# Kernel tuning notes

Hardware: AMD Instinct MI355X
Metric: run time of the kernel (lower is better)

Reference implementation:

```python
import jax, jax.numpy as jnp
import numpy as np

B, T, D_IN, P, Q, D_OUT = 128, 1024, 64, 128, 2, 64


def _lstm_layer(x, w_ih, w_hh, b):
    """One LSTM layer, batch_first. x: [B,T,Din], w_ih: [4P,Din], w_hh: [4P,P], b: [4P].
    PyTorch gate order: i, f, g, o."""
    # Precompute input contribution for all timesteps (the big, parallel GEMM).
    gx = jnp.einsum('btd,gd->btg', x, w_ih) + b          # [B,T,4P]
    gx_t = jnp.swapaxes(gx, 0, 1)                        # [T,B,4P] for scan
    p = w_hh.shape[1]
    h0 = jnp.zeros((x.shape[0], p), dtype=x.dtype)
    c0 = jnp.zeros((x.shape[0], p), dtype=x.dtype)

    def step(carry, g_in):
        h, c = carry
        g = g_in + h @ w_hh.T                            # [B,4P]
        i, f, gg, o = jnp.split(g, 4, axis=-1)
        i = jax.nn.sigmoid(i)
        f = jax.nn.sigmoid(f)
        gg = jnp.tanh(gg)
        o = jax.nn.sigmoid(o)
        c = f * c + i * gg
        h = o * jnp.tanh(c)
        return (h, c), h

    _, hs = jax.lax.scan(step, (h0, c0), gx_t)           # hs: [T,B,P]
    return jnp.swapaxes(hs, 0, 1)                        # [B,T,P]


def setup_inputs() -> dict:
    key = jax.random.key(0)
    ks = jax.random.split(key, 8)
    x = jax.random.normal(ks[0], (B, T, D_IN), dtype=jnp.float32)
    # weight_ih: kaiming-normal-ish; weight_hh: orthogonal-ish (random normal is a fine stand-in
    # numerically; init distribution doesn't change the math being tested).
    w_ih0 = jax.random.normal(ks[1], (4 * P, D_IN), dtype=jnp.float32) * (1.0 / np.sqrt(D_IN))
    w_hh0 = jax.random.normal(ks[2], (4 * P, P), dtype=jnp.float32) * (1.0 / np.sqrt(P))
    w_ih1 = jax.random.normal(ks[3], (4 * P, P), dtype=jnp.float32) * (1.0 / np.sqrt(P))
    w_hh1 = jax.random.normal(ks[4], (4 * P, P), dtype=jnp.float32) * (1.0 / np.sqrt(P))
    # biases initialized to zero in the original (bias_ih + bias_hh folded into one per layer
    # would be equivalent math; keep both for faithfulness)
    b_ih = jnp.zeros((Q, 4 * P), dtype=jnp.float32)
    b_hh = jnp.zeros((Q, 4 * P), dtype=jnp.float32)
    fc_w = jax.random.normal(ks[5], (D_OUT, P), dtype=jnp.float32) * np.sqrt(2.0 / P)
    fc_b = jnp.zeros((D_OUT,), dtype=jnp.float32)
    return {"x": x, "w_ih0": w_ih0, "w_hh0": w_hh0, "w_ih1": w_ih1, "w_hh1": w_hh1,
            "b_ih": b_ih, "b_hh": b_hh, "fc_w": fc_w, "fc_b": fc_b}


def reference(x, w_ih0, w_hh0, w_ih1, w_hh1, b_ih, b_hh, fc_w, fc_b):
    h = _lstm_layer(x, w_ih0, w_hh0, b_ih[0] + b_hh[0])   # layer 0: [B,T,P]
    h = _lstm_layer(h, w_ih1, w_hh1, b_ih[1] + b_hh[1])   # layer 1: [B,T,P]
    return jnp.einsum('btp,op->bto', h, fc_w) + fc_b      # [B,T,D_OUT]
```

## Files before the change

kernel.cpp:

```cpp
#include <hip/hip_runtime.h>

#define NT 1024
#define RINGS 256

typedef _Float16 half8 __attribute__((ext_vector_type(8)));
typedef _Float16 half4 __attribute__((ext_vector_type(4)));
typedef float f32x4 __attribute__((ext_vector_type(4)));
typedef unsigned long long u64;
struct U2 { u64 a, b; };

#ifndef __has_builtin
#define __has_builtin(x) 0
#endif

__device__ __forceinline__ f32x4 MFMA(half8 a, half8 b, f32x4 c) {
  return __builtin_amdgcn_mfma_f32_16x16x32_f16(a, b, c, 0, 0, 0);
}
__device__ __forceinline__ float exp2h(float x) {
#if __has_builtin(__builtin_amdgcn_exp2f)
  return __builtin_amdgcn_exp2f(x);
#else
  return exp2f(x);
#endif
}
__device__ __forceinline__ float sigf(float x) {
  return __builtin_amdgcn_rcpf(1.0f + exp2h(x * -1.44269504f));
}
__device__ __forceinline__ float tanhf2(float x) {
  float t = __builtin_amdgcn_rcpf(1.0f + exp2h(x * 2.88539008f));
  return fmaf(-2.0f, t, 1.0f);
}
__device__ __forceinline__ half8 cvt8(float4 c0, float4 c1) {
  half8 hv;
  hv[0] = (_Float16)c0.x; hv[1] = (_Float16)c0.y;
  hv[2] = (_Float16)c0.z; hv[3] = (_Float16)c0.w;
  hv[4] = (_Float16)c1.x; hv[5] = (_Float16)c1.y;
  hv[6] = (_Float16)c1.z; hv[7] = (_Float16)c1.w;
  return hv;
}
__device__ __forceinline__ half8 ldring(const _Float16* p) {
  const u64* q = (const u64*)p;
  U2 uu;
  uu.a = __hip_atomic_load(q, __ATOMIC_RELAXED, __HIP_MEMORY_SCOPE_AGENT);
  uu.b = __hip_atomic_load(q + 1, __ATOMIC_RELAXED, __HIP_MEMORY_SCOPE_AGENT);
  return __builtin_bit_cast(half8, uu);
}
__device__ __forceinline__ unsigned wpoll(unsigned* p, unsigned tgt,
                                          unsigned cached, int l) {
  unsigned c = cached;
  while (c < tgt) {
    unsigned pv = 0;
    if (l == 0)
      pv = __hip_atomic_load(p, __ATOMIC_ACQUIRE, __HIP_MEMORY_SCOPE_AGENT);
    c = (unsigned)__builtin_amdgcn_readfirstlane((int)pv);
    if (c < tgt) __builtin_amdgcn_s_sleep(2);
  }
  return c;
}

__global__ __launch_bounds__(256) void prep_x(const float* __restrict__ x,
                                              _Float16* __restrict__ Xf) {
  int t0 = blockIdx.x * 256 + threadIdx.x;
  int l = t0 & 63;
  int fid = t0 >> 6;
  int kt = fid & 1;
  int t = (fid >> 1) & (NT - 1);
  int g = fid >> 11;
  int bt = g * 16 + (l & 15);
  int kb = kt * 32 + (l >> 4) * 4;
  const float* src = x + ((size_t)bt * NT + (size_t)t) * 64 + kb;
  float4 v0 = *(const float4*)src;
  float4 v1 = *(const float4*)(src + 16);
  *(half8*)(Xf + (size_t)fid * 512 + l * 8) = cvt8(v0, v1);
}

__global__ __launch_bounds__(512, 1) void lstm_main(
    const float* __restrict__ wih0, const float* __restrict__ whh0,
    const float* __restrict__ wih1, const float* __restrict__ whh1,
    const float* __restrict__ bih, const float* __restrict__ bhh,
    const float* __restrict__ fcw, const float* __restrict__ fcb,
    const _Float16* __restrict__ Xf, _Float16* __restrict__ ringH0,
    unsigned* __restrict__ flags, float* __restrict__ out) {
  const int tid = threadIdx.x;
  const int w = tid >> 6, l = tid & 63;
  const int n = l & 15, lg = l >> 4;
  const bool producer = blockIdx.x < 8;
  const int g = blockIdx.x & 7;

  __shared__ _Float16 hfr[2][4][64][8];
  __shared__ _Float16 fcl[4][4][64][8];

  _Float16* ringG = ringH0 + (size_t)g * RINGS * 2048;
  unsigned* prog = flags + g * 16;
  unsigned* cons = flags + (8 + g) * 16;
  const half8 hz = {0, 0, 0, 0, 0, 0, 0, 0};

  if (producer) {
    half8 A[4][6];
    f32x4 bias[4];
#pragma unroll
    for (int q = 0; q < 4; ++q) {
      int row = (w + 8 * q) * 16 + n;
#pragma unroll
      for (int kt = 0; kt < 2; ++kt) {
        const float* wp = wih0 + (size_t)row * 64 + kt * 32 + lg * 4;
        A[q][kt] = cvt8(*(const float4*)wp, *(const float4*)(wp + 16));
      }
#pragma unroll
      for (int kt = 0; kt < 4; ++kt) {
        const float* wp = whh0 + (size_t)row * 128 + kt * 32 + lg * 4;
        A[q][2 + kt] = cvt8(*(const float4*)wp, *(const float4*)(wp + 16));
      }
      int rb = (w + 8 * q) * 16 + lg * 4;
      f32x4 bv;
#pragma unroll
      for (int r = 0; r < 4; ++r) bv[r] = bih[rb + r] + bhh[rb + r];
      bias[q] = bv;
    }
    if (tid < 256) ((half8*)&hfr[1][0][0][0])[tid] = hz;
    const _Float16* XfG = Xf + (size_t)g * NT * 1024;
    half8 x0 = *(const half8*)(XfG + l * 8);
    half8 x1 = *(const half8*)(XfG + 512 + l * 8);
    f32x4 cst = {0.f, 0.f, 0.f, 0.f};
    unsigned Cc = 0;
    __syncthreads();
    for (int s = 0; s < NT; ++s) {
      half8 xn0, xn1;
      if (s + 1 < NT) {
        const _Float16* p = XfG + (size_t)(s + 1) * 1024 + l * 8;
        xn0 = *(const half8*)p;
        xn1 = *(const half8*)(p + 512);
      }
      if (s >= 224 && (s & 31) == 0)
        Cc = wpoll(cons, (unsigned)(s - 192), Cc, l);
      const int rdk = (s + 1) & 1;
      half8 b2 = *(const half8*)&hfr[rdk][0][l][0];
      half8 b3 = *(const half8*)&hfr[rdk][1][l][0];
      half8 b4 = *(const half8*)&hfr[rdk][2][l][0];
      half8 b5 = *(const half8*)&hfr[rdk][3][l][0];
      f32x4 xc0 = {0.f, 0.f, 0.f, 0.f}, xc1 = xc0, xc2 = xc0, xc3 = xc0;
      xc0 = MFMA(A[0][0], x0, xc0); xc1 = MFMA(A[1][0], x0, xc1);
      xc2 = MFMA(A[2][0], x0, xc2); xc3 = MFMA(A[3][0], x0, xc3);
      xc0 = MFMA(A[0][1], x1, xc0); xc1 = MFMA(A[1][1], x1, xc1);
      xc2 = MFMA(A[2][1], x1, xc2); xc3 = MFMA(A[3][1], x1, xc3);
      f32x4 hc0 = bias[0], hc1 = bias[1], hc2 = bias[2], hc3 = bias[3];
      hc0 = MFMA(A[0][2], b2, hc0); hc1 = MFMA(A[1][2], b2, hc1);
      hc2 = MFMA(A[2][2], b2, hc2); hc3 = MFMA(A[3][2], b2, hc3);
      hc0 = MFMA(A[0][3], b3, hc0); hc1 = MFMA(A[1][3], b3, hc1);
      hc2 = MFMA(A[2][3], b3, hc2); hc3 = MFMA(A[3][3], b3, hc3);
      hc0 = MFMA(A[0][4], b4, hc0); hc1 = MFMA(A[1][4], b4, hc1);
      hc2 = MFMA(A[2][4], b4, hc2); hc3 = MFMA(A[3][4], b4, hc3);
      hc0 = MFMA(A[0][5], b5, hc0); hc1 = MFMA(A[1][5], b5, hc1);
      hc2 = MFMA(A[2][5], b5, hc2); hc3 = MFMA(A[3][5], b5, hc3);
      f32x4 acc0 = hc0 + xc0, acc1 = hc1 + xc1;
      f32x4 acc2 = hc2 + xc2, acc3 = hc3 + xc3;
      half4 hh;
#pragma unroll
      for (int r = 0; r < 4; ++r) {
        float iv = sigf(acc0[r]), fv = sigf(acc1[r]);
        float gv = tanhf2(acc2[r]), ov = sigf(acc3[r]);
        cst[r] = fv * cst[r] + iv * gv;
        hh[r] = (_Float16)(ov * tanhf2(cst[r]));
      }
      *(half4*)&hfr[s & 1][w >> 1][l][(w & 1) << 2] = hh;
      {
        u64 uh = __builtin_bit_cast(u64, hh);
        __hip_atomic_store(
            (u64*)(ringG + (size_t)(s & (RINGS - 1)) * 2048 +
                   (w >> 1) * 512 + l * 8 + (w & 1) * 4),
            uh, __ATOMIC_RELAXED, __HIP_MEMORY_SCOPE_AGENT);
      }
      asm volatile("s_waitcnt lgkmcnt(0)" ::: "memory");
      __builtin_amdgcn_sched_barrier(0);
      __builtin_amdgcn_s_barrier();
      __builtin_amdgcn_sched_barrier(0);
      if ((s & 31) == 31) {
        asm volatile("s_waitcnt vmcnt(0)" ::: "memory");
        __builtin_amdgcn_sched_barrier(0);
        __builtin_amdgcn_s_barrier();
        __builtin_amdgcn_sched_barrier(0);
        if (tid == 0)
          __hip_atomic_store(prog, (unsigned)(s + 1), __ATOMIC_RELEASE,
                             __HIP_MEMORY_SCOPE_AGENT);
      }
      x0 = xn0;
      x1 = xn1;
    }
  } else {
    half8 A[4][8];
    f32x4 bias[4], fcbv = {0.f, 0.f, 0.f, 0.f};
#pragma unroll
    for (int q = 0; q < 4; ++q) {
      int row = (w + 8 * q) * 16 + n;
#pragma unroll
      for (int kt = 0; kt < 4; ++kt) {
        const float* wp = wih1 + (size_t)row * 128 + kt * 32 + lg * 4;
        A[q][kt] = cvt8(*(const float4*)wp, *(const float4*)(wp + 16));
      }
#pragma unroll
      for (int kt = 0; kt < 4; ++kt) {
        const float* wp = whh1 + (size_t)row * 128 + kt * 32 + lg * 4;
        A[q][4 + kt] = cvt8(*(const float4*)wp, *(const float4*)(wp + 16));
      }
      int rb = (w + 8 * q) * 16 + lg * 4;
      f32x4 bv;
#pragma unroll
      for (int r = 0; r < 4; ++r)
        bv[r] = bih[512 + rb + r] + bhh[512 + rb + r];
      bias[q] = bv;
    }
    if (w < 4) {
      int frow = (w << 4) + n;
#pragma unroll
      for (int kt = 0; kt < 4; ++kt) {
        const float* wp = fcw + (size_t)frow * 128 + kt * 32 + lg * 4;
        *(half8*)&fcl[w][kt][l][0] =
            cvt8(*(const float4*)wp, *(const float4*)(wp + 16));
      }
      fcbv = *(const f32x4*)(fcb + (w << 4) + lg * 4);
    }
    if (tid < 256) ((half8*)&hfr[1][0][0][0])[tid] = hz;
    float* outG = out + (size_t)((g << 4) + n) * NT * 64 + (w << 4) + lg * 4;
    f32x4 cst = {0.f, 0.f, 0.f, 0.f};
    __syncthreads();
    unsigned Pc = wpoll(prog, 2u, 0u, l);
    half8 hA0 = ldring(ringG + l * 8);
    half8 hA1 = ldring(ringG + 512 + l * 8);
    half8 hA2 = ldring(ringG + 1024 + l * 8);
    half8 hA3 = ldring(ringG + 1536 + l * 8);
    const _Float16* rb1 = ringG + 2048 + l * 8;
    half8 hB0 = ldring(rb1);
    half8 hB1 = ldring(rb1 + 512);
    half8 hB2 = ldring(rb1 + 1024);
    half8 hB3 = ldring(rb1 + 1536);

#define CSTEP(T, C0, C1, C2, C3)                                               \
  {                                                                            \
    const int rdk_ = ((T) + 1) & 1;                                            \
    half8 b4 = *(const half8*)&hfr[rdk_][0][l][0];                             \
    half8 b5 = *(const half8*)&hfr[rdk_][1][l][0];                             \
    half8 b6 = *(const half8*)&hfr[rdk_][2][l][0];                             \
    half8 b7 = *(const half8*)&hfr[rdk_][3][l][0];                             \
                      \
    f32x4 ic0 = {0.f, 0.f, 0.f, 0.f}, ic1 = ic0, ic2 = ic0, ic3 = ic0;         \
    ic0 = MFMA(A[0][0], C0, ic0); ic1 = MFMA(A[1][0], C0, ic1);                \
    ic2 = MFMA(A[2][0], C0, ic2); ic3 = MFMA(A[3][0], C0, ic3);                \
    ic0 = MFMA(A[0][1], C1, ic0); ic1 = MFMA(A[1][1], C1, ic1);                \
    ic2 = MFMA(A[2][1], C1, ic2); ic3 = MFMA(A[3][1], C1, ic3);                \
    ic0 = MFMA(A[0][2], C2, ic0); ic1 = MFMA(A[1][2], C2, ic1);                \
    ic2 = MFMA(A[2][2], C2, ic2); ic3 = MFMA(A[3][2], C2, ic3);                \
    ic0 = MFMA(A[0][3], C3, ic0); ic1 = MFMA(A[1][3], C3, ic1);                \
    ic2 = MFMA(A[2][3], C3, ic2); ic3 = MFMA(A[3][3], C3, ic3);                \
    if ((T) + 2 < NT) {    \
      Pc = wpoll(prog, (unsigned)((T) + 3), Pc, l);                            \
      const _Float16* rb_ =                                                    \
          ringG + (size_t)(((T) + 2) & (RINGS - 1)) * 2048 + l * 8;            \
      C0 = ldring(rb_);        C1 = ldring(rb_ + 512);                         \
      C2 = ldring(rb_ + 1024); C3 = ldring(rb_ + 1536);                        \
    }                                                                          \
                                                   \
    f32x4 hc0 = bias[0], hc1 = bias[1], hc2 = bias[2], hc3 = bias[3];          \
    hc0 = MFMA(A[0][4], b4, hc0); hc1 = MFMA(A[1][4], b4, hc1);                \
    hc2 = MFMA(A[2][4], b4, hc2); hc3 = MFMA(A[3][4], b4, hc3);                \
    hc0 = MFMA(A[0][5], b5, hc0); hc1 = MFMA(A[1][5], b5, hc1);                \
    hc2 = MFMA(A[2][5], b5, hc2); hc3 = MFMA(A[3][5], b5, hc3);                \
    hc0 = MFMA(A[0][6], b6, hc0); hc1 = MFMA(A[1][6], b6, hc1);                \
    hc2 = MFMA(A[2][6], b6, hc2); hc3 = MFMA(A[3][6], b6, hc3);                \
    hc0 = MFMA(A[0][7], b7, hc0); hc1 = MFMA(A[1][7], b7, hc1);                \
    hc2 = MFMA(A[2][7], b7, hc2); hc3 = MFMA(A[3][7], b7, hc3);                \
    if (w < 4) {                           \
      half8 f0 = *(const half8*)&fcl[w][0][l][0];                              \
      half8 f1 = *(const half8*)&fcl[w][1][l][0];                              \
      half8 f2 = *(const half8*)&fcl[w][2][l][0];                              \
      half8 f3 = *(const half8*)&fcl[w][3][l][0];                              \
      f32x4 afc = fcbv;                                                        \
      afc = MFMA(f0, b4, afc); afc = MFMA(f1, b5, afc);                        \
      afc = MFMA(f2, b6, afc); afc = MFMA(f3, b7, afc);                        \
      if ((T) >= 1) *(f32x4*)(outG + (size_t)((T) - 1) * 64) = afc;            \
    }                                                                          \
    f32x4 acc0 = hc0 + ic0, acc1 = hc1 + ic1;                                  \
    f32x4 acc2 = hc2 + ic2, acc3 = hc3 + ic3;                                  \
    half4 hh;                                                                  \
    _Pragma("unroll")                                                          \
    for (int r = 0; r < 4; ++r) {                                              \
      float iv = sigf(acc0[r]), fv = sigf(acc1[r]);                            \
      float gv = tanhf2(acc2[r]), ov = sigf(acc3[r]);                          \
      cst[r] = fv * cst[r] + iv * gv;                                          \
      hh[r] = (_Float16)(ov * tanhf2(cst[r]));                                 \
    }                                                                          \
    *(half4*)&hfr[(T) & 1][w >> 1][l][(w & 1) << 2] = hh;                      \
    if (tid == 0 && ((T) & 31) == 0)                                           \
      __hip_atomic_store(cons, (unsigned)(T), __ATOMIC_RELAXED,                \
                         __HIP_MEMORY_SCOPE_AGENT);                            \
    asm volatile("s_waitcnt lgkmcnt(0)" ::: "memory");                         \
    __builtin_amdgcn_sched_barrier(0);                                         \
    __builtin_amdgcn_s_barrier();             \
    __builtin_amdgcn_sched_barrier(0);                                         \
  }

    for (int t = 0; t < NT; t += 2) {
      CSTEP(t, hA0, hA1, hA2, hA3);
      CSTEP(t + 1, hB0, hB1, hB2, hB3);
    }
#undef CSTEP
    {
      half8 b4 = *(const half8*)&hfr[(NT + 1) & 1][0][l][0];
      half8 b5 = *(const half8*)&hfr[(NT + 1) & 1][1][l][0];
      half8 b6 = *(const half8*)&hfr[(NT + 1) & 1][2][l][0];
      half8 b7 = *(const half8*)&hfr[(NT + 1) & 1][3][l][0];
      if (w < 4) {
        half8 f0 = *(const half8*)&fcl[w][0][l][0];
        half8 f1 = *(const half8*)&fcl[w][1][l][0];
        half8 f2 = *(const half8*)&fcl[w][2][l][0];
        half8 f3 = *(const half8*)&fcl[w][3][l][0];
        f32x4 afc = fcbv;
        afc = MFMA(f0, b4, afc); afc = MFMA(f1, b5, afc);
        afc = MFMA(f2, b6, afc); afc = MFMA(f3, b7, afc);
        *(f32x4*)(outG + (size_t)(NT - 1) * 64) = afc;
      }
    }
  }
}

extern "C" void kernel_launch(void* const* d_in, const int* in_sizes, int n_in,
                              void* d_out, int out_size, void* d_ws, size_t ws_size,
                              hipStream_t stream) {
  const float* x     = (const float*)d_in[0];
  const float* w_ih0 = (const float*)d_in[1];
  const float* w_hh0 = (const float*)d_in[2];
  const float* w_ih1 = (const float*)d_in[3];
  const float* w_hh1 = (const float*)d_in[4];
  const float* b_ih  = (const float*)d_in[5];
  const float* b_hh  = (const float*)d_in[6];
  const float* fc_w  = (const float*)d_in[7];
  const float* fc_b  = (const float*)d_in[8];

  _Float16* Xf   = (_Float16*)d_ws;
  _Float16* ring = (_Float16*)((char*)d_ws + (16u << 20));
  unsigned* flags = (unsigned*)((char*)d_ws + (24u << 20));

  hipMemsetAsync(flags, 0, 4096, stream);
  prep_x<<<4096, 256, 0, stream>>>(x, Xf);
  lstm_main<<<16, 512, 0, stream>>>(w_ih0, w_hh0, w_ih1, w_hh1, b_ih, b_hh,
                                    fc_w, fc_b, Xf, ring, flags,
                                    (float*)d_out);
}
```

Baseline: 1.337 ms.

## Offload input projections to a third block role feeding both recurrences

Adds a third group of 8 blocks that computes the input-gate projections for layer 0 (from x) and layer 1 (from layer-0 hidden states) and streams them to fp32 ring buffers in global memory with progress flags. The two recurrent roles then only perform the hidden-to-hidden MFMAs plus gate math on their serial critical path, loading precomputed gate inputs two steps ahead. The aim is to shorten the per-timestep latency of the sequential recurrence. In exchange it adds extra global traffic and more inter-block flag polling, and it changes the synchronisation cadence to every 8 steps.

```diff
diff --git a/kernel.cpp b/kernel.cpp
--- a/kernel.cpp
+++ b/kernel.cpp
@@ -1,13 +1,14 @@
 #include <hip/hip_runtime.h>
 
 #define NT 1024
-#define RINGS 256
+#define H0S 256
+#define GS 64
+#define LAG 32
 
 typedef _Float16 half8 __attribute__((ext_vector_type(8)));
 typedef _Float16 half4 __attribute__((ext_vector_type(4)));
 typedef float f32x4 __attribute__((ext_vector_type(4)));
 typedef unsigned long long u64;
-struct U2 { u64 a, b; };
 
 #ifndef __has_builtin
 #define __has_builtin(x) 0
@@ -37,13 +38,6 @@
   hv[4] = (_Float16)c1.x; hv[5] = (_Float16)c1.y;
   hv[6] = (_Float16)c1.z; hv[7] = (_Float16)c1.w;
   return hv;
-}
-__device__ __forceinline__ half8 ldring(const _Float16* p) {
-  const u64* q = (const u64*)p;
-  U2 uu;
-  uu.a = __hip_atomic_load(q, __ATOMIC_RELAXED, __HIP_MEMORY_SCOPE_AGENT);
-  uu.b = __hip_atomic_load(q + 1, __ATOMIC_RELAXED, __HIP_MEMORY_SCOPE_AGENT);
-  return __builtin_bit_cast(half8, uu);
 }
 __device__ __forceinline__ unsigned wpoll(unsigned* p, unsigned tgt,
                                           unsigned cached, int l) {
@@ -57,6 +51,18 @@
   }
   return c;
 }
+
+#define DRAIN_BARRIER()                              \
+  asm volatile("s_waitcnt vmcnt(0)" ::: "memory");   \
+  __builtin_amdgcn_sched_barrier(0);                 \
+  __builtin_amdgcn_s_barrier();                      \
+  __builtin_amdgcn_sched_barrier(0)
+
+#define LGKM_BARRIER()                               \
+  asm volatile("s_waitcnt lgkmcnt(0)" ::: "memory"); \
+  __builtin_amdgcn_sched_barrier(0);                 \
+  __builtin_amdgcn_s_barrier();                      \
+  __builtin_amdgcn_sched_barrier(0)
 
 __global__ __launch_bounds__(256) void prep_x(const float* __restrict__ x,
                                               _Float16* __restrict__ Xf) {
@@ -79,243 +85,302 @@
     const float* __restrict__ wih1, const float* __restrict__ whh1,
     const float* __restrict__ bih, const float* __restrict__ bhh,
     const float* __restrict__ fcw, const float* __restrict__ fcb,
-    const _Float16* __restrict__ Xf, _Float16* __restrict__ ringH0,
+    const _Float16* __restrict__ Xf, _Float16* __restrict__ h0R,
+    float* __restrict__ gxR, float* __restrict__ gyR,
     unsigned* __restrict__ flags, float* __restrict__ out) {
   const int tid = threadIdx.x;
   const int w = tid >> 6, l = tid & 63;
   const int n = l & 15, lg = l >> 4;
-  const bool producer = blockIdx.x < 8;
+  const int role = blockIdx.x >> 3;
   const int g = blockIdx.x & 7;
 
   __shared__ _Float16 hfr[2][4][64][8];
-  __shared__ _Float16 fcl[4][4][64][8];
-
-  _Float16* ringG = ringH0 + (size_t)g * RINGS * 2048;
-  unsigned* prog = flags + g * 16;
-  unsigned* cons = flags + (8 + g) * 16;
+
+  _Float16* h0G = h0R + (size_t)g * H0S * 2048;
+  float* gxG = gxR + (size_t)g * GS * 8192;
+  float* gyG = gyR + (size_t)g * GS * 8192;
+  unsigned* pX  = flags + (0 * 8 + g) * 16;
+  unsigned* pXY = flags + (1 * 8 + g) * 16;
+  unsigned* pP  = flags + (2 * 8 + g) * 16;
+  unsigned* pY  = flags + (3 * 8 + g) * 16;
   const half8 hz = {0, 0, 0, 0, 0, 0, 0, 0};
 
-  if (producer) {
-    half8 A[4][6];
-    f32x4 bias[4];
+  if (role == 0) {
+    half8 Ax[4][2], Ai[4][4];
+    f32x4 b0v[4], b1v[4];
 #pragma unroll
     for (int q = 0; q < 4; ++q) {
       int row = (w + 8 * q) * 16 + n;
 #pragma unroll
       for (int kt = 0; kt < 2; ++kt) {
         const float* wp = wih0 + (size_t)row * 64 + kt * 32 + lg * 4;
-        A[q][kt] = cvt8(*(const float4*)wp, *(const float4*)(wp + 16));
-      }
+        Ax[q][kt] = cvt8(*(const float4*)wp, *(const float4*)(wp + 16));
+      }
+#pragma unroll
+      for (int kt = 0; kt < 4; ++kt) {
+        const float* wp = wih1 + (size_t)row * 128 + kt * 32 + lg * 4;
+        Ai[q][kt] = cvt8(*(const float4*)wp, *(const float4*)(wp + 16));
+      }
+      int rb = (w + 8 * q) * 16 + lg * 4;
+      f32x4 v0, v1;
+#pragma unroll
+      for (int r = 0; r < 4; ++r) {
+        v0[r] = bih[rb + r] + bhh[rb + r];
+        v1[r] = bih[512 + rb + r] + bhh[512 + rb + r];
+      }
+      b0v[q] = v0;
+      b1v[q] = v1;
+    }
+    const _Float16* XfG = Xf + (size_t)g * NT * 1024;
+    half8 xv0 = *(const half8*)(XfG + l * 8);
+    half8 xv1 = *(const half8*)(XfG + 512 + l * 8);
+    half8 hb0 = hz, hb1 = hz, hb2 = hz, hb3 = hz;
+    unsigned Pp = 0, Yp = 0;
+    for (int s = 0; s < NT + LAG; ++s) {
+      const int u = s - LAG;
+      if (s < NT) {
+        f32x4 a0 = MFMA(Ax[0][0], xv0, b0v[0]);
+        f32x4 a1 = MFMA(Ax[1][0], xv0, b0v[1]);
+        f32x4 a2 = MFMA(Ax[2][0], xv0, b0v[2]);
+        f32x4 a3 = MFMA(Ax[3][0], xv0, b0v[3]);
+        a0 = MFMA(Ax[0][1], xv1, a0); a1 = MFMA(Ax[1][1], xv1, a1);
+        a2 = MFMA(Ax[2][1], xv1, a2); a3 = MFMA(Ax[3][1], xv1, a3);
+        float* gp = gxG + (size_t)(s & (GS - 1)) * 8192;
+        *(f32x4*)(gp + ((0 + w) * 64 + l) * 4) = a0;
+        *(f32x4*)(gp + ((8 + w) * 64 + l) * 4) = a1;
+        *(f32x4*)(gp + ((16 + w) * 64 + l) * 4) = a2;
+        *(f32x4*)(gp + ((24 + w) * 64 + l) * 4) = a3;
+        if (s + 1 < NT) {
+          const _Float16* p = XfG + (size_t)(s + 1) * 1024 + l * 8;
+          xv0 = *(const half8*)p;
+          xv1 = *(const half8*)(p + 512);
+        }
+      }
+      if (u >= 0) {
+        if (u == 0) {
+          Pp = wpoll(pP, 1u, Pp, l);
+          const _Float16* hp = h0G + l * 8;
+          hb0 = *(const half8*)hp;
+          hb1 = *(const half8*)(hp + 512);
+          hb2 = *(const half8*)(hp + 1024);
+          hb3 = *(const half8*)(hp + 1536);
+        }
+        f32x4 c0 = MFMA(Ai[0][0], hb0, b1v[0]);
+        f32x4 c1 = MFMA(Ai[1][0], hb0, b1v[1]);
+        f32x4 c2 = MFMA(Ai[2][0], hb0, b1v[2]);
+        f32x4 c3 = MFMA(Ai[3][0], hb0, b1v[3]);
+        c0 = MFMA(Ai[0][1], hb1, c0); c1 = MFMA(Ai[1][1], hb1, c1);
+        c2 = MFMA(Ai[2][1], hb1, c2); c3 = MFMA(Ai[3][1], hb1, c3);
+        c0 = MFMA(Ai[0][2], hb2, c0); c1 = MFMA(Ai[1][2], hb2, c1);
+        c2 = MFMA(Ai[2][2], hb2, c2); c3 = MFMA(Ai[3][2], hb2, c3);
+        c0 = MFMA(Ai[0][3], hb3, c0); c1 = MFMA(Ai[1][3], hb3, c1);
+        c2 = MFMA(Ai[2][3], hb3, c2); c3 = MFMA(Ai[3][3], hb3, c3);
+        float* gp = gyG + (size_t)(u & (GS - 1)) * 8192;
+        *(f32x4*)(gp + ((0 + w) * 64 + l) * 4) = c0;
+        *(f32x4*)(gp + ((8 + w) * 64 + l) * 4) = c1;
+        *(f32x4*)(gp + ((16 + w) * 64 + l) * 4) = c2;
+        *(f32x4*)(gp + ((24 + w) * 64 + l) * 4) = c3;
+        if (u + 1 < NT) {
+          Pp = wpoll(pP, (unsigned)(u + 2), Pp, l);
+          const _Float16* hp =
+              h0G + (size_t)((u + 1) & (H0S - 1)) * 2048 + l * 8;
+          hb0 = *(const half8*)hp;
+          hb1 = *(const half8*)(hp + 512);
+          hb2 = *(const half8*)(hp + 1024);
+          hb3 = *(const half8*)(hp + 1536);
+        }
+        if ((u & 15) == 0 && u >= 56)
+          Yp = wpoll(pY, (unsigned)(u - 48), Yp, l);
+      }
+      if ((s & 7) == 7) {
+        DRAIN_BARRIER();
+        if (tid == 0) {
+          __hip_atomic_store(pX, (unsigned)(s + 1), __ATOMIC_RELEASE,
+                             __HIP_MEMORY_SCOPE_AGENT);
+          if (u >= 0)
+            __hip_atomic_store(pXY, (unsigned)(u + 1), __ATOMIC_RELEASE,
+                               __HIP_MEMORY_SCOPE_AGENT);
+        }
+      }
+    }
+    DRAIN_BARRIER();
+    if (tid == 0) {
+      __hip_atomic_store(pX, (unsigned)(NT + LAG), __ATOMIC_RELEASE,
+                         __HIP_MEMORY_SCOPE_AGENT);
+      __hip_atomic_store(pXY, (unsigned)(NT + LAG), __ATOMIC_RELEASE,
+                         __HIP_MEMORY_SCOPE_AGENT);
+    }
+  } else if (role == 1) {
+    half8 Ah[4][4];
+#pragma unroll
+    for (int q = 0; q < 4; ++q) {
+      int row = (w + 8 * q) * 16 + n;
 #pragma unroll
       for (int kt = 0; kt < 4; ++kt) {
         const float* wp = whh0 + (size_t)row * 128 + kt * 32 + lg * 4;
-        A[q][2 + kt] = cvt8(*(const float4*)wp, *(const float4*)(wp + 16));
-      }
-      int rb = (w + 8 * q) * 16 + lg * 4;
-      f32x4 bv;
-#pragma unroll
-      for (int r = 0; r < 4; ++r) bv[r] = bih[rb + r] + bhh[rb + r];
-      bias[q] = bv;
+        Ah[q][kt] = cvt8(*(const float4*)wp, *(const float4*)(wp + 16));
+      }
     }
     if (tid < 256) ((half8*)&hfr[1][0][0][0])[tid] = hz;
-    const _Float16* XfG = Xf + (size_t)g * NT * 1024;
-    half8 x0 = *(const half8*)(XfG + l * 8);
-    half8 x1 = *(const half8*)(XfG + 512 + l * 8);
     f32x4 cst = {0.f, 0.f, 0.f, 0.f};
-    unsigned Cc = 0;
+    unsigned Xp = wpoll(pX, 2u, 0u, l);
+    f32x4 gA0 = *(const f32x4*)(gxG + ((0 + w) * 64 + l) * 4);
+    f32x4 gA1 = *(const f32x4*)(gxG + ((8 + w) * 64 + l) * 4);
+    f32x4 gA2 = *(const f32x4*)(gxG + ((16 + w) * 64 + l) * 4);
+    f32x4 gA3 = *(const f32x4*)(gxG + ((24 + w) * 64 + l) * 4);
+    const float* g1 = gxG + 8192;
+    f32x4 gB0 = *(const f32x4*)(g1 + ((0 + w) * 64 + l) * 4);
+    f32x4 gB1 = *(const f32x4*)(g1 + ((8 + w) * 64 + l) * 4);
+    f32x4 gB2 = *(const f32x4*)(g1 + ((16 + w) * 64 + l) * 4);
+    f32x4 gB3 = *(const f32x4*)(g1 + ((24 + w) * 64 + l) * 4);
     __syncthreads();
-    for (int s = 0; s < NT; ++s) {
-      half8 xn0, xn1;
-      if (s + 1 < NT) {
-        const _Float16* p = XfG + (size_t)(s + 1) * 1024 + l * 8;
-        xn0 = *(const half8*)p;
-        xn1 = *(const half8*)(p + 512);
-      }
-      if (s >= 224 && (s & 31) == 0)
-        Cc = wpoll(cons, (unsigned)(s - 192), Cc, l);
-      const int rdk = (s + 1) & 1;
-      half8 b2 = *(const half8*)&hfr[rdk][0][l][0];
-      half8 b3 = *(const half8*)&hfr[rdk][1][l][0];
-      half8 b4 = *(const half8*)&hfr[rdk][2][l][0];
-      half8 b5 = *(const half8*)&hfr[rdk][3][l][0];
-      f32x4 xc0 = {0.f, 0.f, 0.f, 0.f}, xc1 = xc0, xc2 = xc0, xc3 = xc0;
-      xc0 = MFMA(A[0][0], x0, xc0); xc1 = MFMA(A[1][0], x0, xc1);
-      xc2 = MFMA(A[2][0], x0, xc2); xc3 = MFMA(A[3][0], x0, xc3);
-      xc0 = MFMA(A[0][1], x1, xc0); xc1 = MFMA(A[1][1], x1, xc1);
-      xc2 = MFMA(A[2][1], x1, xc2); xc3 = MFMA(A[3][1], x1, xc3);
-      f32x4 hc0 = bias[0], hc1 = bias[1], hc2 = bias[2], hc3 = bias[3];
-      hc0 = MFMA(A[0][2], b2, hc0); hc1 = MFMA(A[1][2], b2, hc1);
-      hc2 = MFMA(A[2][2], b2, hc2); hc3 = MFMA(A[3][2], b2, hc3);
-      hc0 = MFMA(A[0][3], b3, hc0); hc1 = MFMA(A[1][3], b3, hc1);
-      hc2 = MFMA(A[2][3], b3, hc2); hc3 = MFMA(A[3][3], b3, hc3);
-      hc0 = MFMA(A[0][4], b4, hc0); hc1 = MFMA(A[1][4], b4, hc1);
-      hc2 = MFMA(A[2][4], b4, hc2); hc3 = MFMA(A[3][4], b4, hc3);
-      hc0 = MFMA(A[0][5], b5, hc0); hc1 = MFMA(A[1][5], b5, hc1);
-      hc2 = MFMA(A[2][5], b5, hc2); hc3 = MFMA(A[3][5], b5, hc3);
-      f32x4 acc0 = hc0 + xc0, acc1 = hc1 + xc1;
-      f32x4 acc2 = hc2 + xc2, acc3 = hc3 + xc3;
-      half4 hh;
-#pragma unroll
-      for (int r = 0; r < 4; ++r) {
-        float iv = sigf(acc0[r]), fv = sigf(acc1[r]);
-        float gv = tanhf2(acc2[r]), ov = sigf(acc3[r]);
-        cst[r] = fv * cst[r] + iv * gv;
-        hh[r] = (_Float16)(ov * tanhf2(cst[r]));
-      }
-      *(half4*)&hfr[s & 1][w >> 1][l][(w & 1) << 2] = hh;
-      {
-        u64 uh = __builtin_bit_cast(u64, hh);
-        __hip_atomic_store(
-            (u64*)(ringG + (size_t)(s & (RINGS - 1)) * 2048 +
-                   (w >> 1) * 512 + l * 8 + (w & 1) * 4),
-            uh, __ATOMIC_RELAXED, __HIP_MEMORY_SCOPE_AGENT);
-      }
-      asm volatile("s_waitcnt lgkmcnt(0)" ::: "memory");
-      __builtin_amdgcn_sched_barrier(0);
-      __builtin_amdgcn_s_barrier();
-      __builtin_amdgcn_sched_barrier(0);
-      if ((s & 31) == 31) {
-        asm volatile("s_waitcnt vmcnt(0)" ::: "memory");
-        __builtin_amdgcn_sched_barrier(0);
-        __builtin_amdgcn_s_barrier();
-        __builtin_amdgcn_sched_barrier(0);
-        if (tid == 0)
-          __hip_atomic_store(prog, (unsigned)(s + 1), __ATOMIC_RELEASE,
-                             __HIP_MEMORY_SCOPE_AGENT);
-      }
-      x0 = xn0;
-      x1 = xn1;
-    }
+
+#define PSTEP(T, G0, G1, G2, G3)                                               \
+  {                                                                            \
+    const int rdk_ = ((T) + 1) & 1;                                            \
+    half8 b0 = *(const half8*)&hfr[rdk_][0][l][0];                             \
+    half8 b1 = *(const half8*)&hfr[rdk_][1][l][0];                             \
+    half8 b2 = *(const half8*)&hfr[rdk_][2][l][0];                             \
+    half8 b3 = *(const half8*)&hfr[rdk_][3][l][0];                             \
+    f32x4 c0 = G0, c1 = G1, c2 = G2, c3 = G3;                                  \
+    c0 = MFMA(Ah[0][0], b0, c0); c1 = MFMA(Ah[1][0], b0, c1);                  \
+    c2 = MFMA(Ah[2][0], b0, c2); c3 = MFMA(Ah[3][0], b0, c3);                  \
+    c0 = MFMA(Ah[0][1], b1, c0); c1 = MFMA(Ah[1][1], b1, c1);                  \
+    c2 = MFMA(Ah[2][1], b1, c2); c3 = MFMA(Ah[3][1], b1, c3);                  \
+    c0 = MFMA(Ah[0][2], b2, c0); c1 = MFMA(Ah[1][2], b2, c1);                  \
+    c2 = MFMA(Ah[2][2], b2, c2); c3 = MFMA(Ah[3][2], b2, c3);                  \
+    c0 = MFMA(Ah[0][3], b3, c0); c1 = MFMA(Ah[1][3], b3, c1);                  \
+    c2 = MFMA(Ah[2][3], b3, c2); c3 = MFMA(Ah[3][3], b3, c3);                  \
+    if ((T) + 2 < NT) {      \
+      Xp = wpoll(pX, (unsigned)((T) + 3), Xp, l);                              \
+      const float* gp_ = gxG + (size_t)(((T) + 2) & (GS - 1)) * 8192;          \
+      G0 = *(const f32x4*)(gp_ + ((0 + w) * 64 + l) * 4);                      \
+      G1 = *(const f32x4*)(gp_ + ((8 + w) * 64 + l) * 4);                      \
+      G2 = *(const f32x4*)(gp_ + ((16 + w) * 64 + l) * 4);                     \
+      G3 = *(const f32x4*)(gp_ + ((24 + w) * 64 + l) * 4);                     \
+    }                                                                          \
+    half4 hh;                                                                  \
+    _Pragma("unroll")                                                          \
+    for (int r = 0; r < 4; ++r) {                                              \
+      float iv = sigf(c0[r]), fv = sigf(c1[r]);                                \
+      float gv = tanhf2(c2[r]), ov = sigf(c3[r]);                              \
+      cst[r] = fv * cst[r] + iv * gv;                                          \
+      hh[r] = (_Float16)(ov * tanhf2(cst[r]));                                 \
+    }                                                                          \
+    *(half4*)&hfr[(T) & 1][w >> 1][l][(w & 1) << 2] = hh;                      \
+    *(u64*)(h0G + (size_t)((T) & (H0S - 1)) * 2048 + (w >> 1) * 512 + l * 8 +  \
+            (w & 1) * 4) = __builtin_bit_cast(u64, hh);                        \
+    LGKM_BARRIER();                                                            \
+    if (((T) & 7) == 7) {                                                      \
+      DRAIN_BARRIER();                                                         \
+      if (tid == 0)                                                            \
+        __hip_atomic_store(pP, (unsigned)((T) + 1), __ATOMIC_RELEASE,          \
+                           __HIP_MEMORY_SCOPE_AGENT);                          \
+    }                                                                          \
+  }
+
+    for (int s = 0; s < NT; s += 2) {
+      PSTEP(s, gA0, gA1, gA2, gA3);
+      PSTEP(s + 1, gB0, gB1, gB2, gB3);
+    }
+#undef PSTEP
   } else {
-    half8 A[4][8];
-    f32x4 bias[4], fcbv = {0.f, 0.f, 0.f, 0.f};
+    half8 Ah[4][4], FCA[4];
+    f32x4 fcbv = {0.f, 0.f, 0.f, 0.f};
 #pragma unroll
     for (int q = 0; q < 4; ++q) {
       int row = (w + 8 * q) * 16 + n;
 #pragma unroll
       for (int kt = 0; kt < 4; ++kt) {
-        const float* wp = wih1 + (size_t)row * 128 + kt * 32 + lg * 4;
-        A[q][kt] = cvt8(*(const float4*)wp, *(const float4*)(wp + 16));
-      }
-#pragma unroll
-      for (int kt = 0; kt < 4; ++kt) {
         const float* wp = whh1 + (size_t)row * 128 + kt * 32 + lg * 4;
-        A[q][4 + kt] = cvt8(*(const float4*)wp, *(const float4*)(wp + 16));
-      }
-      int rb = (w + 8 * q) * 16 + lg * 4;
-      f32x4 bv;
-#pragma unroll
-      for (int r = 0; r < 4; ++r)
-        bv[r] = bih[512 + rb + r] + bhh[512 + rb + r];
-      bias[q] = bv;
-    }
-    if (w < 4) {
+        Ah[q][kt] = cvt8(*(const float4*)wp, *(const float4*)(wp + 16));
+      }
+    }
+    const bool fcon = (w < 4);
+    if (fcon) {
       int frow = (w << 4) + n;
 #pragma unroll
       for (int kt = 0; kt < 4; ++kt) {
         const float* wp = fcw + (size_t)frow * 128 + kt * 32 + lg * 4;
-        *(half8*)&fcl[w][kt][l][0] =
-            cvt8(*(const float4*)wp, *(const float4*)(wp + 16));
+        FCA[kt] = cvt8(*(const float4*)wp, *(const float4*)(wp + 16));
       }
       fcbv = *(const f32x4*)(fcb + (w << 4) + lg * 4);
     }
     if (tid < 256) ((half8*)&hfr[1][0][0][0])[tid] = hz;
     float* outG = out + (size_t)((g << 4) + n) * NT * 64 + (w << 4) + lg * 4;
     f32x4 cst = {0.f, 0.f, 0.f, 0.f};
+    unsigned XYp = wpoll(pXY, 2u, 0u, l);
+    f32x4 gA0 = *(const f32x4*)(gyG + ((0 + w) * 64 + l) * 4);
+    f32x4 gA1 = *(const f32x4*)(gyG + ((8 + w) * 64 + l) * 4);
+    f32x4 gA2 = *(const f32x4*)(gyG + ((16 + w) * 64 + l) * 4);
+    f32x4 gA3 = *(const f32x4*)(gyG + ((24 + w) * 64 + l) * 4);
+    const float* g1 = gyG + 8192;
+    f32x4 gB0 = *(const f32x4*)(g1 + ((0 + w) * 64 + l) * 4);
+    f32x4 gB1 = *(const f32x4*)(g1 + ((8 + w) * 64 + l) * 4);
+    f32x4 gB2 = *(const f32x4*)(g1 + ((16 + w) * 64 + l) * 4);
+    f32x4 gB3 = *(const f32x4*)(g1 + ((24 + w) * 64 + l) * 4);
     __syncthreads();
-    unsigned Pc = wpoll(prog, 2u, 0u, l);
-    half8 hA0 = ldring(ringG + l * 8);
-    half8 hA1 = ldring(ringG + 512 + l * 8);
-    half8 hA2 = ldring(ringG + 1024 + l * 8);
-    half8 hA3 = ldring(ringG + 1536 + l * 8);
-    const _Float16* rb1 = ringG + 2048 + l * 8;
-    half8 hB0 = ldring(rb1);
-    half8 hB1 = ldring(rb1 + 512);
-    half8 hB2 = ldring(rb1 + 1024);
-    half8 hB3 = ldring(rb1 + 1536);
-
-#define CSTEP(T, C0, C1, C2, C3)                                               \
+
+#define YSTEP(T, G0, G1, G2, G3)                                               \
   {                                                                            \
     const int rdk_ = ((T) + 1) & 1;                                            \
-    half8 b4 = *(const half8*)&hfr[rdk_][0][l][0];                             \
-    half8 b5 = *(const half8*)&hfr[rdk_][1][l][0];                             \
-    half8 b6 = *(const half8*)&hfr[rdk_][2][l][0];                             \
-    half8 b7 = *(const half8*)&hfr[rdk_][3][l][0];                             \
-                      \
-    f32x4 ic0 = {0.f, 0.f, 0.f, 0.f}, ic1 = ic0, ic2 = ic0, ic3 = ic0;         \
-    ic0 = MFMA(A[0][0], C0, ic0); ic1 = MFMA(A[1][0], C0, ic1);                \
-    ic2 = MFMA(A[2][0], C0, ic2); ic3 = MFMA(A[3][0], C0, ic3);                \
-    ic0 = MFMA(A[0][1], C1, ic0); ic1 = MFMA(A[1][1], C1, ic1);                \
-    ic2 = MFMA(A[2][1], C1, ic2); ic3 = MFMA(A[3][1], C1, ic3);                \
-    ic0 = MFMA(A[0][2], C2, ic0); ic1 = MFMA(A[1][2], C2, ic1);                \
-    ic2 = MFMA(A[2][2], C2, ic2); ic3 = MFMA(A[3][2], C2, ic3);                \
-    ic0 = MFMA(A[0][3], C3, ic0); ic1 = MFMA(A[1][3], C3, ic1);                \
-    ic2 = MFMA(A[2][3], C3, ic2); ic3 = MFMA(A[3][3], C3, ic3);                \
-    if ((T) + 2 < NT) {    \
-      Pc = wpoll(prog, (unsigned)((T) + 3), Pc, l);                            \
-      const _Float16* rb_ =                                                    \
-          ringG + (size_t)(((T) + 2) & (RINGS - 1)) * 2048 + l * 8;            \
-      C0 = ldring(rb_);        C1 = ldring(rb_ + 512);                         \
-      C2 = ldring(rb_ + 1024); C3 = ldring(rb_ + 1536);                        \
-    }                                                                          \
-                                                   \
-    f32x4 hc0 = bias[0], hc1 = bias[1], hc2 = bias[2], hc3 = bias[3];          \
-    hc0 = MFMA(A[0][4], b4, hc0); hc1 = MFMA(A[1][4], b4, hc1);                \
-    hc2 = MFMA(A[2][4], b4, hc2); hc3 = MFMA(A[3][4], b4, hc3);                \
-    hc0 = MFMA(A[0][5], b5, hc0); hc1 = MFMA(A[1][5], b5, hc1);                \
-    hc2 = MFMA(A[2][5], b5, hc2); hc3 = MFMA(A[3][5], b5, hc3);                \
-    hc0 = MFMA(A[0][6], b6, hc0); hc1 = MFMA(A[1][6], b6, hc1);                \
-    hc2 = MFMA(A[2][6], b6, hc2); hc3 = MFMA(A[3][6], b6, hc3);                \
-    hc0 = MFMA(A[0][7], b7, hc0); hc1 = MFMA(A[1][7], b7, hc1);                \
-    hc2 = MFMA(A[2][7], b7, hc2); hc3 = MFMA(A[3][7], b7, hc3);                \
-    if (w < 4) {                           \
-      half8 f0 = *(const half8*)&fcl[w][0][l][0];                              \
-      half8 f1 = *(const half8*)&fcl[w][1][l][0];                              \
-      half8 f2 = *(const half8*)&fcl[w][2][l][0];                              \
-      half8 f3 = *(const half8*)&fcl[w][3][l][0];                              \
+    half8 b0 = *(const half8*)&hfr[rdk_][0][l][0];                             \
+    half8 b1 = *(const half8*)&hfr[rdk_][1][l][0];                             \
+    half8 b2 = *(const half8*)&hfr[rdk_][2][l][0];                             \
+    half8 b3 = *(const half8*)&hfr[rdk_][3][l][0];                             \
+    f32x4 c0 = G0, c1 = G1, c2 = G2, c3 = G3;                                  \
+    c0 = MFMA(Ah[0][0], b0, c0); c1 = MFMA(Ah[1][0], b0, c1);                  \
+    c2 = MFMA(Ah[2][0], b0, c2); c3 = MFMA(Ah[3][0], b0, c3);                  \
+    c0 = MFMA(Ah[0][1], b1, c0); c1 = MFMA(Ah[1][1], b1, c1);                  \
+    c2 = MFMA(Ah[2][1], b1, c2); c3 = MFMA(Ah[3][1], b1, c3);                  \
+    c0 = MFMA(Ah[0][2], b2, c0); c1 = MFMA(Ah[1][2], b2, c1);                  \
+    c2 = MFMA(Ah[2][2], b2, c2); c3 = MFMA(Ah[3][2], b2, c3);                  \
+    c0 = MFMA(Ah[0][3], b3, c0); c1 = MFMA(Ah[1][3], b3, c1);                  \
+    c2 = MFMA(Ah[2][3], b3, c2); c3 = MFMA(Ah[3][3], b3, c3);                  \
+    if (fcon) {                                             \
       f32x4 afc = fcbv;                                                        \
-      afc = MFMA(f0, b4, afc); afc = MFMA(f1, b5, afc);                        \
-      afc = MFMA(f2, b6, afc); afc = MFMA(f3, b7, afc);                        \
+      afc = MFMA(FCA[0], b0, afc); afc = MFMA(FCA[1], b1, afc);                \
+      afc = MFMA(FCA[2], b2, afc); afc = MFMA(FCA[3], b3, afc);                \
       if ((T) >= 1) *(f32x4*)(outG + (size_t)((T) - 1) * 64) = afc;            \
     }                                                                          \
-    f32x4 acc0 = hc0 + ic0, acc1 = hc1 + ic1;                                  \
-    f32x4 acc2 = hc2 + ic2, acc3 = hc3 + ic3;                                  \
+    if ((T) + 2 < NT) {                                  \
+      XYp = wpoll(pXY, (unsigned)((T) + 3), XYp, l);                           \
+      const float* gp_ = gyG + (size_t)(((T) + 2) & (GS - 1)) * 8192;          \
+      G0 = *(const f32x4*)(gp_ + ((0 + w) * 64 + l) * 4);                      \
+      G1 = *(const f32x4*)(gp_ + ((8 + w) * 64 + l) * 4);                      \
+      G2 = *(const f32x4*)(gp_ + ((16 + w) * 64 + l) * 4);                     \
+      G3 = *(const f32x4*)(gp_ + ((24 + w) * 64 + l) * 4);                     \
+    }                                                                          \
     half4 hh;                                                                  \
     _Pragma("unroll")                                                          \
     for (int r = 0; r < 4; ++r) {                                              \
-      float iv = sigf(acc0[r]), fv = sigf(acc1[r]);                            \
-      float gv = tanhf2(acc2[r]), ov = sigf(acc3[r]);                          \
+      float iv = sigf(c0[r]), fv = sigf(c1[r]);                                \
+      float gv = tanhf2(c2[r]), ov = sigf(c3[r]);                              \
       cst[r] = fv * cst[r] + iv * gv;                                          \
       hh[r] = (_Float16)(ov * tanhf2(cst[r]));                                 \
     }                                                                          \
     *(half4*)&hfr[(T) & 1][w >> 1][l][(w & 1) << 2] = hh;                      \
-    if (tid == 0 && ((T) & 31) == 0)                                           \
-      __hip_atomic_store(cons, (unsigned)(T), __ATOMIC_RELAXED,                \
+    LGKM_BARRIER();                                                            \
+    if (((T) & 7) == 7 && tid == 0)       \
+      __hip_atomic_store(pY, (unsigned)((T) + 1), __ATOMIC_RELAXED,            \
                          __HIP_MEMORY_SCOPE_AGENT);                            \
-    asm volatile("s_waitcnt lgkmcnt(0)" ::: "memory");                         \
-    __builtin_amdgcn_sched_barrier(0);                                         \
-    __builtin_amdgcn_s_barrier();             \
-    __builtin_amdgcn_sched_barrier(0);                                         \
   }
 
     for (int t = 0; t < NT; t += 2) {
-      CSTEP(t, hA0, hA1, hA2, hA3);
-      CSTEP(t + 1, hB0, hB1, hB2, hB3);
-    }
-#undef CSTEP
+      YSTEP(t, gA0, gA1, gA2, gA3);
+      YSTEP(t + 1, gB0, gB1, gB2, gB3);
+    }
+#undef YSTEP
     {
-      half8 b4 = *(const half8*)&hfr[(NT + 1) & 1][0][l][0];
-      half8 b5 = *(const half8*)&hfr[(NT + 1) & 1][1][l][0];
-      half8 b6 = *(const half8*)&hfr[(NT + 1) & 1][2][l][0];
-      half8 b7 = *(const half8*)&hfr[(NT + 1) & 1][3][l][0];
-      if (w < 4) {
-        half8 f0 = *(const half8*)&fcl[w][0][l][0];
-        half8 f1 = *(const half8*)&fcl[w][1][l][0];
-        half8 f2 = *(const half8*)&fcl[w][2][l][0];
-        half8 f3 = *(const half8*)&fcl[w][3][l][0];
+      const int rdk = (NT + 1) & 1;
+      half8 b0 = *(const half8*)&hfr[rdk][0][l][0];
+      half8 b1 = *(const half8*)&hfr[rdk][1][l][0];
+      half8 b2 = *(const half8*)&hfr[rdk][2][l][0];
+      half8 b3 = *(const half8*)&hfr[rdk][3][l][0];
+      if (fcon) {
         f32x4 afc = fcbv;
-        afc = MFMA(f0, b4, afc); afc = MFMA(f1, b5, afc);
-        afc = MFMA(f2, b6, afc); afc = MFMA(f3, b7, afc);
+        afc = MFMA(FCA[0], b0, afc); afc = MFMA(FCA[1], b1, afc);
+        afc = MFMA(FCA[2], b2, afc); afc = MFMA(FCA[3], b3, afc);
         *(f32x4*)(outG + (size_t)(NT - 1) * 64) = afc;
       }
     }
@@ -335,13 +400,15 @@
   const float* fc_w  = (const float*)d_in[7];
   const float* fc_b  = (const float*)d_in[8];
 
-  _Float16* Xf   = (_Float16*)d_ws;
-  _Float16* ring = (_Float16*)((char*)d_ws + (16u << 20));
-  unsigned* flags = (unsigned*)((char*)d_ws + (24u << 20));
-
-  hipMemsetAsync(flags, 0, 4096, stream);
+  _Float16* Xf  = (_Float16*)d_ws;
+  _Float16* h0R = (_Float16*)((char*)d_ws + (16u << 20));
+  float* gxR    = (float*)((char*)d_ws + (24u << 20));
+  float* gyR    = (float*)((char*)d_ws + (40u << 20));
+  unsigned* flags = (unsigned*)((char*)d_ws + (56u << 20));
+
+  (void)hipMemsetAsync(flags, 0, 4096, stream);
   prep_x<<<4096, 256, 0, stream>>>(x, Xf);
-  lstm_main<<<16, 512, 0, stream>>>(w_ih0, w_hh0, w_ih1, w_hh1, b_ih, b_hh,
-                                    fc_w, fc_b, Xf, ring, flags,
+  lstm_main<<<24, 512, 0, stream>>>(w_ih0, w_hh0, w_ih1, w_hh1, b_ih, b_hh,
+                                    fc_w, fc_b, Xf, h0R, gxR, gyR, flags,
                                     (float*)d_out);
 }
```

After: 1.230 ms (median of 2 runs). 8.1% less time.
